# Kernel tuning notes

Measured on AMD Instinct MI355X. Metric: run time of the kernel, lower is better.

The kernel has to match this reference:

```python
import jax, jax.numpy as jnp
import numpy as np

D_MODEL = 512
NHEAD = 8
D_K = D_MODEL // NHEAD


def setup_inputs() -> dict:
    key = jax.random.key(0)
    ks = jax.random.split(key, 9)
    s = 1.0 / np.sqrt(D_MODEL)
    x = jax.random.normal(ks[0], (2, 2048, D_MODEL), dtype=jnp.float32)
    # torch Linear weights: [out_features, in_features]
    Wq = jax.random.uniform(ks[1], (D_MODEL, D_MODEL), jnp.float32, -s, s)
    bq = jax.random.uniform(ks[2], (D_MODEL,), jnp.float32, -s, s)
    Wk = jax.random.uniform(ks[3], (D_MODEL, D_MODEL), jnp.float32, -s, s)
    bk = jax.random.uniform(ks[4], (D_MODEL,), jnp.float32, -s, s)
    Wv = jax.random.uniform(ks[5], (D_MODEL, D_MODEL), jnp.float32, -s, s)
    bv = jax.random.uniform(ks[6], (D_MODEL,), jnp.float32, -s, s)
    Wo = jax.random.uniform(ks[7], (D_MODEL, D_MODEL), jnp.float32, -s, s)
    bo = jax.random.uniform(ks[8], (D_MODEL,), jnp.float32, -s, s)
    return {"x": x, "Wq": Wq, "bq": bq, "Wk": Wk, "bk": bk,
            "Wv": Wv, "bv": bv, "Wo": Wo, "bo": bo}


def reference(x, Wq, bq, Wk, bk, Wv, bv, Wo, bo):
    B, S, D = x.shape
    H, Dk = NHEAD, D_K

    def proj(W, b):
        # torch Linear: x @ W.T + b -> [B, S, D] -> [B, H, S, Dk]
        y = jnp.einsum('bsd,ed->bse', x, W) + b
        return y.reshape(B, S, H, Dk).transpose(0, 2, 1, 3)

    q = proj(Wq, bq)
    k = proj(Wk, bk)
    v = proj(Wv, bv)

    scores = jnp.einsum('bhqd,bhkd->bhqk', q, k) / jnp.sqrt(jnp.float32(Dk))
    attn = jax.nn.softmax(scores, axis=-1)  # explicit O(S^2) attention matrix
    out = jnp.einsum('bhqk,bhkd->bhqd', attn, v)
    out = out.transpose(0, 2, 1, 3).reshape(B, S, D)
    return jnp.einsum('bsd,ed->bse', out, Wo) + bo
```

## Files before the change

### kernel.cpp

```cpp
#include <hip/hip_runtime.h>

typedef __bf16 bf16_t;
typedef bf16_t bf16x8 __attribute__((ext_vector_type(8)));
typedef bf16_t bf16x4 __attribute__((ext_vector_type(4)));
typedef float  floatx4 __attribute__((ext_vector_type(4)));

#define D_MODEL 512
#define NHEAD   8
#define DK      64
#define BATCH   2
#define SEQ     2048
#define MTOT    (BATCH*SEQ)
#define QSCALE  0.18033688011112042591f

static __device__ __forceinline__ floatx4 mfma16(bf16x8 a, bf16x8 b, floatx4 c) {
    return __builtin_amdgcn_mfma_f32_16x16x32_bf16(a, b, c, 0, 0, 0);
}

__global__ __launch_bounds__(256)
void qkv_proj(const float* __restrict__ x,
              const float* __restrict__ Wq, const float* __restrict__ bq,
              const float* __restrict__ Wk, const float* __restrict__ bk,
              const float* __restrict__ Wv, const float* __restrict__ bv,
              bf16_t* __restrict__ q_ws, bf16_t* __restrict__ k_ws,
              bf16_t* __restrict__ vt_ws)
{
    __shared__ bf16_t Asq[128 * 40];
    __shared__ bf16_t Bsq[128 * 40];

    const int mtile = blockIdx.x;
    const int ntile = blockIdx.y;
    const int which = ntile >> 2;
    const int nsub  = ntile & 3;
    const float* W    = (which == 0) ? Wq : (which == 1) ? Wk : Wv;
    const float* bias = (which == 0) ? bq : (which == 1) ? bk : bv;

    const int tid  = threadIdx.x;
    const int lane = tid & 63;
    const int wave = tid >> 6;
    const int wm = wave & 1, wn = wave >> 1;
    const int l15 = lane & 15, quad = lane >> 4;

    const int m0 = mtile * 128;
    const int n0 = nsub * 128;
    const int srow = tid >> 3;
    const int sseg = tid & 7;

    floatx4 acc[4][4] = {};

    for (int k0 = 0; k0 < 512; k0 += 32) {
        __syncthreads();
        #pragma unroll
        for (int rep = 0; rep < 4; ++rep) {
            const int r = srow + rep * 32;
            const float4 va = *(const float4*)(x + (size_t)(m0 + r) * 512 + k0 + sseg * 4);
            bf16x4 pa; pa[0]=(bf16_t)va.x; pa[1]=(bf16_t)va.y; pa[2]=(bf16_t)va.z; pa[3]=(bf16_t)va.w;
            *(bf16x4*)(&Asq[r * 40 + sseg * 4]) = pa;
            const float4 vb = *(const float4*)(W + (size_t)(n0 + r) * 512 + k0 + sseg * 4);
            bf16x4 pb; pb[0]=(bf16_t)vb.x; pb[1]=(bf16_t)vb.y; pb[2]=(bf16_t)vb.z; pb[3]=(bf16_t)vb.w;
            *(bf16x4*)(&Bsq[r * 40 + sseg * 4]) = pb;
        }
        __syncthreads();

        bf16x8 af[4], bfr[4];
        #pragma unroll
        for (int i = 0; i < 4; ++i)
            af[i] = *(const bf16x8*)(&Asq[(wm * 64 + i * 16 + l15) * 40 + quad * 8]);
        #pragma unroll
        for (int j = 0; j < 4; ++j)
            bfr[j] = *(const bf16x8*)(&Bsq[(wn * 64 + j * 16 + l15) * 40 + quad * 8]);
        #pragma unroll
        for (int i = 0; i < 4; ++i)
            #pragma unroll
            for (int j = 0; j < 4; ++j)
                acc[i][j] = mfma16(af[i], bfr[j], acc[i][j]);
    }

    const float scale = (which == 0) ? QSCALE : 1.0f;
    #pragma unroll
    for (int j = 0; j < 4; ++j) {
        const int e = n0 + wn * 64 + j * 16 + l15;
        const float be = bias[e];
        const int h = e >> 6, d = e & 63;
        #pragma unroll
        for (int i = 0; i < 4; ++i) {
            const int mbase = m0 + wm * 64 + i * 16 + quad * 4;
            const int b = mbase >> 11;
            const int sl = mbase & 2047;
            floatx4 c = acc[i][j];
            if (which == 2) {
                bf16x4 pk;
                #pragma unroll
                for (int r = 0; r < 4; ++r) pk[r] = (bf16_t)(c[r] + be);
                *(bf16x4*)(vt_ws + ((size_t)((b * 8 + h) * 64 + d)) * 2048 + sl) = pk;
            } else {
                bf16_t* dst = (which == 0) ? q_ws : k_ws;
                #pragma unroll
                for (int r = 0; r < 4; ++r)
                    dst[(size_t)(b * 8 + h) * (SEQ * DK) + (size_t)(sl + r) * 64 + d] =
                        (bf16_t)((c[r] + be) * scale);
            }
        }
    }
}

#define SD 88
#define PS 68
__global__ __launch_bounds__(512, 4)
void attn_kernel(const bf16_t* __restrict__ q_ws, const bf16_t* __restrict__ k_ws,
                 const bf16_t* __restrict__ vt_ws, bf16_t* __restrict__ attn_ws)
{
    __shared__ bf16_t Ks [2][64 * SD];
    __shared__ bf16_t Vts[2][64 * SD];
    __shared__ bf16_t Ps [8][16 * PS];

    const int bh = blockIdx.x;
    const int qt = blockIdx.y;
    const int tid = threadIdx.x, lane = tid & 63, wave = tid >> 6;
    const int l15 = lane & 15, quad = lane >> 4;
    const int g  = wave >> 2;
    const int wq = wave & 3;

    const bf16_t* Qb  = q_ws  + (size_t)bh * SEQ * DK;
    const bf16_t* Kb  = k_ws  + (size_t)bh * SEQ * DK;
    const bf16_t* Vtb = vt_ws + (size_t)bh * DK * SEQ;
    bf16_t* Pw = &Ps[wave][0];

    const int srow = tid >> 3;
    const int sseg = tid & 7;

    const int qrow = qt * 64 + wq * 16 + l15;
    const bf16x8 aq0 = *(const bf16x8*)(Qb + (size_t)qrow * 64 + quad * 8);
    const bf16x8 aq1 = *(const bf16x8*)(Qb + (size_t)qrow * 64 + 32 + quad * 8);

    floatx4 O[4] = {};
    float rs[4] = {0.f, 0.f, 0.f, 0.f};

    for (int t = 0; t < 16; ++t) {
        __syncthreads();
        {
            const int kg0 = (2 * t + 0) * 64;
            const int kg1 = (2 * t + 1) * 64;
            *(bf16x8*)(&Ks[0][srow * SD + sseg * 8]) =
                *(const bf16x8*)(Kb + (size_t)(kg0 + srow) * 64 + sseg * 8);
            *(bf16x8*)(&Ks[1][srow * SD + sseg * 8]) =
                *(const bf16x8*)(Kb + (size_t)(kg1 + srow) * 64 + sseg * 8);
            *(bf16x8*)(&Vts[0][srow * SD + sseg * 8]) =
                *(const bf16x8*)(Vtb + (size_t)srow * 2048 + kg0 + sseg * 8);
            *(bf16x8*)(&Vts[1][srow * SD + sseg * 8]) =
                *(const bf16x8*)(Vtb + (size_t)srow * 2048 + kg1 + sseg * 8);
        }
        __syncthreads();

        floatx4 sc[4];
        #pragma unroll
        for (int kf = 0; kf < 4; ++kf) {
            bf16x8 b0 = *(const bf16x8*)(&Ks[g][(kf * 16 + l15) * SD + quad * 8]);
            bf16x8 b1 = *(const bf16x8*)(&Ks[g][(kf * 16 + l15) * SD + 32 + quad * 8]);
            floatx4 z = {0.f, 0.f, 0.f, 0.f};
            z = mfma16(aq0, b0, z);
            z = mfma16(aq1, b1, z);
            sc[kf] = z;
        }

        #pragma unroll
        for (int kf = 0; kf < 4; ++kf)
            #pragma unroll
            for (int r = 0; r < 4; ++r) {
                const float p = __builtin_amdgcn_exp2f(sc[kf][r]);
                rs[r] += p;
                Pw[(quad * 4 + r) * PS + kf * 16 + l15] = (bf16_t)p;
            }
        asm volatile("s_waitcnt lgkmcnt(0)" ::: "memory");

        bf16x4 p0 = *(const bf16x4*)(&Pw[l15 * PS + quad * 8]);
        bf16x4 p1 = *(const bf16x4*)(&Pw[l15 * PS + quad * 8 + 4]);
        bf16x4 p2 = *(const bf16x4*)(&Pw[l15 * PS + 32 + quad * 8]);
        bf16x4 p3 = *(const bf16x4*)(&Pw[l15 * PS + 32 + quad * 8 + 4]);
        bf16x8 ap0 = __builtin_shufflevector(p0, p1, 0, 1, 2, 3, 4, 5, 6, 7);
        bf16x8 ap1 = __builtin_shufflevector(p2, p3, 0, 1, 2, 3, 4, 5, 6, 7);

        #pragma unroll
        for (int df = 0; df < 4; ++df) {
            bf16x8 b0 = *(const bf16x8*)(&Vts[g][(df * 16 + l15) * SD + quad * 8]);
            bf16x8 b1 = *(const bf16x8*)(&Vts[g][(df * 16 + l15) * SD + 32 + quad * 8]);
            O[df] = mfma16(ap0, b0, O[df]);
            O[df] = mfma16(ap1, b1, O[df]);
        }
    }

    float* scratch = (float*)&Ks[0][0];
    __syncthreads();
    if (g == 1) {
        float* s = scratch + (size_t)(wq * 64 + lane) * 20;
        #pragma unroll
        for (int df = 0; df < 4; ++df)
            #pragma unroll
            for (int r = 0; r < 4; ++r) s[df * 4 + r] = O[df][r];
        #pragma unroll
        for (int r = 0; r < 4; ++r) s[16 + r] = rs[r];
    }
    __syncthreads();
    if (g == 0) {
        const float* s = scratch + (size_t)(wq * 64 + lane) * 20;
        #pragma unroll
        for (int df = 0; df < 4; ++df)
            #pragma unroll
            for (int r = 0; r < 4; ++r) O[df][r] += s[df * 4 + r];
        #pragma unroll
        for (int r = 0; r < 4; ++r) rs[r] += s[16 + r];

        #pragma unroll
        for (int off = 1; off < 16; off <<= 1)
            #pragma unroll
            for (int r = 0; r < 4; ++r) rs[r] += __shfl_xor(rs[r], off, 64);

        const int b = bh >> 3, h = bh & 7;
        #pragma unroll
        for (int r = 0; r < 4; ++r) {
            const float rinv = 1.0f / rs[r];
            const int s_ = qt * 64 + wq * 16 + quad * 4 + r;
            const size_t base = ((size_t)b * 2048 + s_) * 512 + h * 64;
            #pragma unroll
            for (int df = 0; df < 4; ++df)
                attn_ws[base + df * 16 + l15] = (bf16_t)(O[df][r] * rinv);
        }
    }
}

__global__ __launch_bounds__(256)
void out_proj(const bf16_t* __restrict__ attn_ws, const float* __restrict__ Wo,
              const float* __restrict__ bo, float* __restrict__ y)
{
    __shared__ bf16_t As[128 * 40];
    __shared__ bf16_t Bs[128 * 40];

    const int mtile = blockIdx.x;
    const int ntile = blockIdx.y;
    const int tid = threadIdx.x, lane = tid & 63, wave = tid >> 6;
    const int wm = wave & 1, wn = wave >> 1;
    const int l15 = lane & 15, quad = lane >> 4;
    const int m0 = mtile * 128;
    const int n0 = ntile * 128;
    const int srow = tid >> 3, sseg = tid & 7;

    floatx4 acc[4][4] = {};

    for (int k0 = 0; k0 < 512; k0 += 32) {
        __syncthreads();
        #pragma unroll
        for (int rep = 0; rep < 2; ++rep) {
            const int chunk = rep * 256 + tid;
            const int row = chunk >> 2;
            const int seg = chunk & 3;
            *(bf16x8*)(&As[row * 40 + seg * 8]) =
                *(const bf16x8*)(attn_ws + (size_t)(m0 + row) * 512 + k0 + seg * 8);
        }
        #pragma unroll
        for (int rep = 0; rep < 4; ++rep) {
            const int r = srow + rep * 32;
            const float4 vb = *(const float4*)(Wo + (size_t)(n0 + r) * 512 + k0 + sseg * 4);
            bf16x4 pb; pb[0]=(bf16_t)vb.x; pb[1]=(bf16_t)vb.y; pb[2]=(bf16_t)vb.z; pb[3]=(bf16_t)vb.w;
            *(bf16x4*)(&Bs[r * 40 + sseg * 4]) = pb;
        }
        __syncthreads();

        bf16x8 af[4], bfr[4];
        #pragma unroll
        for (int i = 0; i < 4; ++i)
            af[i] = *(const bf16x8*)(&As[(wm * 64 + i * 16 + l15) * 40 + quad * 8]);
        #pragma unroll
        for (int j = 0; j < 4; ++j)
            bfr[j] = *(const bf16x8*)(&Bs[(wn * 64 + j * 16 + l15) * 40 + quad * 8]);
        #pragma unroll
        for (int i = 0; i < 4; ++i)
            #pragma unroll
            for (int j = 0; j < 4; ++j)
                acc[i][j] = mfma16(af[i], bfr[j], acc[i][j]);
    }

    #pragma unroll
    for (int j = 0; j < 4; ++j) {
        const int e = n0 + wn * 64 + j * 16 + l15;
        const float be = bo[e];
        #pragma unroll
        for (int i = 0; i < 4; ++i) {
            const int mb = m0 + wm * 64 + i * 16 + quad * 4;
            #pragma unroll
            for (int r = 0; r < 4; ++r)
                y[(size_t)(mb + r) * 512 + e] = acc[i][j][r] + be;
        }
    }
}

extern "C" void kernel_launch(void* const* d_in, const int* in_sizes, int n_in,
                              void* d_out, int out_size, void* d_ws, size_t ws_size,
                              hipStream_t stream) {
    (void)in_sizes; (void)n_in; (void)out_size; (void)ws_size;
    const float* x  = (const float*)d_in[0];
    const float* Wq = (const float*)d_in[1];
    const float* bq = (const float*)d_in[2];
    const float* Wk = (const float*)d_in[3];
    const float* bk = (const float*)d_in[4];
    const float* Wv = (const float*)d_in[5];
    const float* bv = (const float*)d_in[6];
    const float* Wo = (const float*)d_in[7];
    const float* bo = (const float*)d_in[8];

    bf16_t* qws  = (bf16_t*)d_ws;
    bf16_t* kws  = qws  + (size_t)MTOT * D_MODEL;
    bf16_t* vtws = kws  + (size_t)MTOT * D_MODEL;
    bf16_t* aws  = vtws + (size_t)MTOT * D_MODEL;

    qkv_proj   <<<dim3(32, 12), 256, 0, stream>>>(x, Wq, bq, Wk, bk, Wv, bv, qws, kws, vtws);
    attn_kernel<<<dim3(16, 32), 512, 0, stream>>>(qws, kws, vtws, aws);
    out_proj   <<<dim3(32, 4),  256, 0, stream>>>(aws, Wo, bo, (float*)d_out);
}
```

Before: 153.4 us.

## Give each attention wave two 16-row query tiles to reuse K/V fragments

The attention block drops from 8 waves to 4, and each wave now processes 32 query rows as two 16-row MFMA tiles. Each K and V fragment read from LDS therefore feeds twice as many MFMAs, cutting LDS read traffic per unit of compute. Each thread now stages two rows per K/V tile load. The trade-off is fewer waves per block and more registers per thread (doubled accumulators and score tiles), which can lower occupancy and the latency hiding it provides.

```diff
diff --git a/kernel.cpp b/kernel.cpp
--- a/kernel.cpp
+++ b/kernel.cpp
@@ -106,20 +106,20 @@
 
 #define SD 88
 #define PS 68
-__global__ __launch_bounds__(512, 4)
+__global__ __launch_bounds__(256, 2)
 void attn_kernel(const bf16_t* __restrict__ q_ws, const bf16_t* __restrict__ k_ws,
                  const bf16_t* __restrict__ vt_ws, bf16_t* __restrict__ attn_ws)
 {
     __shared__ bf16_t Ks [2][64 * SD];
     __shared__ bf16_t Vts[2][64 * SD];
-    __shared__ bf16_t Ps [8][16 * PS];
+    __shared__ bf16_t Ps [4][32 * PS];
 
     const int bh = blockIdx.x;
     const int qt = blockIdx.y;
     const int tid = threadIdx.x, lane = tid & 63, wave = tid >> 6;
     const int l15 = lane & 15, quad = lane >> 4;
-    const int g  = wave >> 2;
-    const int wq = wave & 3;
+    const int g  = wave >> 1;
+    const int wq = wave & 1;
 
     const bf16_t* Qb  = q_ws  + (size_t)bh * SEQ * DK;
     const bf16_t* Kb  = k_ws  + (size_t)bh * SEQ * DK;
@@ -129,102 +129,132 @@
     const int srow = tid >> 3;
     const int sseg = tid & 7;
 
-    const int qrow = qt * 64 + wq * 16 + l15;
-    const bf16x8 aq0 = *(const bf16x8*)(Qb + (size_t)qrow * 64 + quad * 8);
-    const bf16x8 aq1 = *(const bf16x8*)(Qb + (size_t)qrow * 64 + 32 + quad * 8);
-
-    floatx4 O[4] = {};
-    float rs[4] = {0.f, 0.f, 0.f, 0.f};
+    bf16x8 aq[2][2];
+    #pragma unroll
+    for (int mt = 0; mt < 2; ++mt)
+        #pragma unroll
+        for (int c = 0; c < 2; ++c)
+            aq[mt][c] = *(const bf16x8*)(Qb +
+                (size_t)(qt * 64 + wq * 32 + mt * 16 + l15) * 64 + c * 32 + quad * 8);
+
+    floatx4 O[2][4] = {};
+    float rs[2][4] = {};
 
     for (int t = 0; t < 16; ++t) {
         __syncthreads();
         {
             const int kg0 = (2 * t + 0) * 64;
             const int kg1 = (2 * t + 1) * 64;
-            *(bf16x8*)(&Ks[0][srow * SD + sseg * 8]) =
-                *(const bf16x8*)(Kb + (size_t)(kg0 + srow) * 64 + sseg * 8);
-            *(bf16x8*)(&Ks[1][srow * SD + sseg * 8]) =
-                *(const bf16x8*)(Kb + (size_t)(kg1 + srow) * 64 + sseg * 8);
-            *(bf16x8*)(&Vts[0][srow * SD + sseg * 8]) =
-                *(const bf16x8*)(Vtb + (size_t)srow * 2048 + kg0 + sseg * 8);
-            *(bf16x8*)(&Vts[1][srow * SD + sseg * 8]) =
-                *(const bf16x8*)(Vtb + (size_t)srow * 2048 + kg1 + sseg * 8);
-        }
-        __syncthreads();
-
-        floatx4 sc[4];
+            #pragma unroll
+            for (int rep = 0; rep < 2; ++rep) {
+                const int row = srow + rep * 32;
+                *(bf16x8*)(&Ks[0][row * SD + sseg * 8]) =
+                    *(const bf16x8*)(Kb + (size_t)(kg0 + row) * 64 + sseg * 8);
+                *(bf16x8*)(&Ks[1][row * SD + sseg * 8]) =
+                    *(const bf16x8*)(Kb + (size_t)(kg1 + row) * 64 + sseg * 8);
+                *(bf16x8*)(&Vts[0][row * SD + sseg * 8]) =
+                    *(const bf16x8*)(Vtb + (size_t)row * 2048 + kg0 + sseg * 8);
+                *(bf16x8*)(&Vts[1][row * SD + sseg * 8]) =
+                    *(const bf16x8*)(Vtb + (size_t)row * 2048 + kg1 + sseg * 8);
+            }
+        }
+        __syncthreads();
+
+        floatx4 sc[2][4];
         #pragma unroll
         for (int kf = 0; kf < 4; ++kf) {
             bf16x8 b0 = *(const bf16x8*)(&Ks[g][(kf * 16 + l15) * SD + quad * 8]);
             bf16x8 b1 = *(const bf16x8*)(&Ks[g][(kf * 16 + l15) * SD + 32 + quad * 8]);
-            floatx4 z = {0.f, 0.f, 0.f, 0.f};
-            z = mfma16(aq0, b0, z);
-            z = mfma16(aq1, b1, z);
-            sc[kf] = z;
-        }
-
-        #pragma unroll
-        for (int kf = 0; kf < 4; ++kf)
-            #pragma unroll
-            for (int r = 0; r < 4; ++r) {
-                const float p = __builtin_amdgcn_exp2f(sc[kf][r]);
-                rs[r] += p;
-                Pw[(quad * 4 + r) * PS + kf * 16 + l15] = (bf16_t)p;
-            }
+            #pragma unroll
+            for (int mt = 0; mt < 2; ++mt) {
+                floatx4 z = {0.f, 0.f, 0.f, 0.f};
+                z = mfma16(aq[mt][0], b0, z);
+                z = mfma16(aq[mt][1], b1, z);
+                sc[mt][kf] = z;
+            }
+        }
+
+        #pragma unroll
+        for (int mt = 0; mt < 2; ++mt)
+            #pragma unroll
+            for (int kf = 0; kf < 4; ++kf)
+                #pragma unroll
+                for (int r = 0; r < 4; ++r) {
+                    const float p = __builtin_amdgcn_exp2f(sc[mt][kf][r]);
+                    rs[mt][r] += p;
+                    Pw[(mt * 16 + quad * 4 + r) * PS + kf * 16 + l15] = (bf16_t)p;
+                }
         asm volatile("s_waitcnt lgkmcnt(0)" ::: "memory");
 
-        bf16x4 p0 = *(const bf16x4*)(&Pw[l15 * PS + quad * 8]);
-        bf16x4 p1 = *(const bf16x4*)(&Pw[l15 * PS + quad * 8 + 4]);
-        bf16x4 p2 = *(const bf16x4*)(&Pw[l15 * PS + 32 + quad * 8]);
-        bf16x4 p3 = *(const bf16x4*)(&Pw[l15 * PS + 32 + quad * 8 + 4]);
-        bf16x8 ap0 = __builtin_shufflevector(p0, p1, 0, 1, 2, 3, 4, 5, 6, 7);
-        bf16x8 ap1 = __builtin_shufflevector(p2, p3, 0, 1, 2, 3, 4, 5, 6, 7);
+        bf16x8 ap[2][2];
+        #pragma unroll
+        for (int mt = 0; mt < 2; ++mt) {
+            bf16x4 p0 = *(const bf16x4*)(&Pw[(mt * 16 + l15) * PS + quad * 8]);
+            bf16x4 p1 = *(const bf16x4*)(&Pw[(mt * 16 + l15) * PS + quad * 8 + 4]);
+            bf16x4 p2 = *(const bf16x4*)(&Pw[(mt * 16 + l15) * PS + 32 + quad * 8]);
+            bf16x4 p3 = *(const bf16x4*)(&Pw[(mt * 16 + l15) * PS + 32 + quad * 8 + 4]);
+            ap[mt][0] = __builtin_shufflevector(p0, p1, 0, 1, 2, 3, 4, 5, 6, 7);
+            ap[mt][1] = __builtin_shufflevector(p2, p3, 0, 1, 2, 3, 4, 5, 6, 7);
+        }
 
         #pragma unroll
         for (int df = 0; df < 4; ++df) {
             bf16x8 b0 = *(const bf16x8*)(&Vts[g][(df * 16 + l15) * SD + quad * 8]);
             bf16x8 b1 = *(const bf16x8*)(&Vts[g][(df * 16 + l15) * SD + 32 + quad * 8]);
-            O[df] = mfma16(ap0, b0, O[df]);
-            O[df] = mfma16(ap1, b1, O[df]);
+            #pragma unroll
+            for (int mt = 0; mt < 2; ++mt) {
+                O[mt][df] = mfma16(ap[mt][0], b0, O[mt][df]);
+                O[mt][df] = mfma16(ap[mt][1], b1, O[mt][df]);
+            }
         }
     }
 
     float* scratch = (float*)&Ks[0][0];
     __syncthreads();
     if (g == 1) {
-        float* s = scratch + (size_t)(wq * 64 + lane) * 20;
-        #pragma unroll
-        for (int df = 0; df < 4; ++df)
-            #pragma unroll
-            for (int r = 0; r < 4; ++r) s[df * 4 + r] = O[df][r];
-        #pragma unroll
-        for (int r = 0; r < 4; ++r) s[16 + r] = rs[r];
+        float* s = scratch + (size_t)(wq * 64 + lane) * 41;
+        #pragma unroll
+        for (int mt = 0; mt < 2; ++mt) {
+            #pragma unroll
+            for (int df = 0; df < 4; ++df)
+                #pragma unroll
+                for (int r = 0; r < 4; ++r) s[mt * 16 + df * 4 + r] = O[mt][df][r];
+            #pragma unroll
+            for (int r = 0; r < 4; ++r) s[32 + mt * 4 + r] = rs[mt][r];
+        }
     }
     __syncthreads();
     if (g == 0) {
-        const float* s = scratch + (size_t)(wq * 64 + lane) * 20;
-        #pragma unroll
-        for (int df = 0; df < 4; ++df)
-            #pragma unroll
-            for (int r = 0; r < 4; ++r) O[df][r] += s[df * 4 + r];
-        #pragma unroll
-        for (int r = 0; r < 4; ++r) rs[r] += s[16 + r];
+        const float* s = scratch + (size_t)(wq * 64 + lane) * 41;
+        #pragma unroll
+        for (int mt = 0; mt < 2; ++mt) {
+            #pragma unroll
+            for (int df = 0; df < 4; ++df)
+                #pragma unroll
+                for (int r = 0; r < 4; ++r) O[mt][df][r] += s[mt * 16 + df * 4 + r];
+            #pragma unroll
+            for (int r = 0; r < 4; ++r) rs[mt][r] += s[32 + mt * 4 + r];
+        }
 
         #pragma unroll
         for (int off = 1; off < 16; off <<= 1)
             #pragma unroll
-            for (int r = 0; r < 4; ++r) rs[r] += __shfl_xor(rs[r], off, 64);
+            for (int mt = 0; mt < 2; ++mt)
+                #pragma unroll
+                for (int r = 0; r < 4; ++r) rs[mt][r] += __shfl_xor(rs[mt][r], off, 64);
 
         const int b = bh >> 3, h = bh & 7;
         #pragma unroll
-        for (int r = 0; r < 4; ++r) {
-            const float rinv = 1.0f / rs[r];
-            const int s_ = qt * 64 + wq * 16 + quad * 4 + r;
-            const size_t base = ((size_t)b * 2048 + s_) * 512 + h * 64;
-            #pragma unroll
-            for (int df = 0; df < 4; ++df)
-                attn_ws[base + df * 16 + l15] = (bf16_t)(O[df][r] * rinv);
-        }
+        for (int mt = 0; mt < 2; ++mt)
+            #pragma unroll
+            for (int r = 0; r < 4; ++r) {
+                const float rinv = 1.0f / rs[mt][r];
+                const int s_ = qt * 64 + wq * 32 + mt * 16 + quad * 4 + r;
+                const size_t base = ((size_t)b * 2048 + s_) * 512 + h * 64;
+                #pragma unroll
+                for (int df = 0; df < 4; ++df)
+                    attn_ws[base + df * 16 + l15] = (bf16_t)(O[mt][df][r] * rinv);
+            }
     }
 }
 
@@ -313,6 +343,6 @@
     bf16_t* aws  = vtws + (size_t)MTOT * D_MODEL;
 
     qkv_proj   <<<dim3(32, 12), 256, 0, stream>>>(x, Wq, bq, Wk, bk, Wv, bv, qws, kws, vtws);
-    attn_kernel<<<dim3(16, 32), 512, 0, stream>>>(qws, kws, vtws, aws);
+    attn_kernel<<<dim3(16, 32), 256, 0, stream>>>(qws, kws, vtws, aws);
     out_proj   <<<dim3(32, 4),  256, 0, stream>>>(aws, Wo, bo, (float*)d_out);
 }
```

Result: no change. 151.8 us (-1.1%).
